# Kernel tuning notes

Measured on AMD Instinct MI355X. Metric: run time of the kernel, lower is better.

The kernel has to match this reference:

```python
import jax, jax.numpy as jnp
import numpy as np
import math


def setup_inputs() -> dict:
    key = jax.random.key(0)
    k1, k2, k3, k4 = jax.random.split(key, 4)
    B, L, H, D = 2, 4096, 8, 64
    factor = 5
    U = factor * int(np.ceil(np.log(L)))  # 45 = sample_k = n_top
    return {
        "queries": jax.random.normal(k1, (B, L, H, D), dtype=jnp.float32),
        "keys": jax.random.normal(k2, (B, L, H, D), dtype=jnp.float32),
        "values": jax.random.normal(k3, (B, L, H, D), dtype=jnp.float32),
        "index_sample": jax.random.randint(k4, (L, U), 0, L),  # sampled key ids per query
    }


def reference(queries, keys, values, index_sample):
    # ProbAttention forward, mask_flag=False (non-causal ProbSparse attention).
    B, L_Q, H, D = queries.shape
    L_K = keys.shape[1]
    Q = jnp.transpose(queries, (0, 2, 1, 3))  # (B,H,L_Q,D)
    K = jnp.transpose(keys, (0, 2, 1, 3))     # (B,H,L_K,D)
    V = jnp.transpose(values, (0, 2, 1, 3))   # (B,H,L_K,D)
    n_top = index_sample.shape[1]             # U = factor*ceil(ln(L_K)) = sample_k = n_top

    # --- _prob_QK: score each query against a random subset of keys ---
    K_sample = K[:, :, index_sample, :]                     # (B,H,L_Q,sample_k,D)
    Q_K_sample = jnp.einsum('bhqd,bhqsd->bhqs', Q, K_sample)
    # sparsity measure M = max - mean (sum divided by full L_K, as in source)
    M = Q_K_sample.max(-1) - Q_K_sample.sum(-1) / L_K       # (B,H,L_Q)
    _, M_top = jax.lax.top_k(M, n_top)                      # (B,H,n_top)

    # full attention scores only for the selected top queries
    Q_reduce = jnp.take_along_axis(Q, M_top[..., None], axis=2)  # (B,H,n_top,D)
    scale = 1.0 / math.sqrt(D)
    scores = jnp.einsum('bhud,bhkd->bhuk', Q_reduce, K) * scale  # (B,H,n_top,L_K)
    attn = jax.nn.softmax(scores, axis=-1)

    # --- initial context (mask_flag=False): cumulative sum of V ---
    context = jnp.cumsum(V, axis=2)                         # (B,H,L_Q,D)

    # --- scatter attention outputs into the top-query rows ---
    update = jnp.einsum('bhuk,bhkd->bhud', attn, V)         # (B,H,n_top,D)
    bi = jnp.arange(B)[:, None, None]
    hi = jnp.arange(H)[None, :, None]
    context = context.at[bi, hi, M_top].set(update)

    return jnp.transpose(context, (0, 2, 1, 3))             # (B,L_Q,H,D)
```

## Files before the change

### kernel.cpp

```cpp
#include <hip/hip_runtime.h>
#include <math.h>

#define BB 2
#define LL 4096
#define HH 8
#define DD 64
#define UU 45
#define TILE 128
#define NTILES (LL / TILE)

#define NC 64
#define CK (LL / NC)
#define KSTR 68
#define SSTR 68

__device__ __forceinline__ int qkv_idx(int b, int l, int h, int d) {
    return ((b * LL + l) * HH + h) * DD + d;
}

__global__ __launch_bounds__(256) void k_computeM(
        const float* __restrict__ Q, const float* __restrict__ K,
        const int* __restrict__ idx, float* __restrict__ M) {
    int w = (blockIdx.x * blockDim.x + threadIdx.x) >> 6;
    int lane = threadIdx.x & 63;
    int q = w % LL;
    int bh = w / LL;
    int h = bh % HH, b = bh / HH;

    const float* Kbh = K + (size_t)(b * LL * HH + h) * DD;
    const size_t rowStride = (size_t)HH * DD;

    float qv = Q[qkv_idx(b, q, h, lane)];
    int myks = idx[q * UU + (lane < UU ? lane : 0)];

    int r = lane >> 4;
    int c16 = lane & 15;

    float q0 = __shfl(qv, c16 * 4 + 0, 64);
    float q1 = __shfl(qv, c16 * 4 + 1, 64);
    float q2 = __shfl(qv, c16 * 4 + 2, 64);
    float q3 = __shfl(qv, c16 * 4 + 3, 64);

    float mval = -INFINITY, sval = 0.f;
#pragma unroll
    for (int g = 0; g < 12; ++g) {
        int s = g * 4 + r;
        int ks = __shfl(myks, s, 64);
        const float4* kp = (const float4*)(Kbh + (size_t)ks * rowStride);
        float4 kk = kp[c16];
        float part = fmaf(kk.x, q0, fmaf(kk.y, q1, fmaf(kk.z, q2, kk.w * q3)));
        part += __shfl_xor(part, 8, 64);
        part += __shfl_xor(part, 4, 64);
        part += __shfl_xor(part, 2, 64);
        part += __shfl_xor(part, 1, 64);
        if (s < UU) { mval = fmaxf(mval, part); sval += part; }
    }
    mval = fmaxf(mval, __shfl_xor(mval, 16, 64));
    sval += __shfl_xor(sval, 16, 64);
    mval = fmaxf(mval, __shfl_xor(mval, 32, 64));
    sval += __shfl_xor(sval, 32, 64);
    if (lane == 0) M[bh * LL + q] = mval - sval * (1.0f / LL);
}

__global__ __launch_bounds__(1024) void k_topk(
        const float* __restrict__ M, int* __restrict__ Mtop) {
    int bh = blockIdx.x;
    int t = threadIdx.x;
    __shared__ unsigned keys[LL];
    __shared__ unsigned hist[256];
    __shared__ unsigned scanbuf[256];
    __shared__ unsigned sPrefix, sMask, sK, sBin;
    __shared__ int outCount, eqCount;
    __shared__ int eqIdx[64];

    for (int i = t; i < LL; i += 1024) {
        unsigned u = __float_as_uint(M[bh * LL + i]);
        keys[i] = (u & 0x80000000u) ? ~u : (u | 0x80000000u);
    }
    if (t == 0) { sPrefix = 0u; sMask = 0u; sK = UU; outCount = 0; eqCount = 0; }
    __syncthreads();

    for (int pass = 0; pass < 4; ++pass) {
        int shift = 24 - pass * 8;
        if (t < 256) hist[t] = 0u;
        __syncthreads();
        unsigned prefix = sPrefix, mask = sMask;
        for (int i = t; i < LL; i += 1024) {
            unsigned k = keys[i];
            if ((k & mask) == prefix)
                atomicAdd(&hist[(k >> shift) & 0xFFu], 1u);
        }
        __syncthreads();
        if (t < 256) scanbuf[t] = hist[t];
        __syncthreads();
        for (int off = 1; off < 256; off <<= 1) {
            unsigned v = 0u;
            if (t < 256 && t + off < 256) v = scanbuf[t + off];
            __syncthreads();
            if (t < 256) scanbuf[t] += v;
            __syncthreads();
        }
        if (t < 256) {
            unsigned k = sK;
            unsigned geq = scanbuf[t];
            unsigned gt = (t < 255) ? scanbuf[t + 1] : 0u;
            if (gt < k && geq >= k) sBin = (unsigned)t;
        }
        __syncthreads();
        if (t == 0) {
            unsigned b = sBin;
            unsigned gt = (b < 255u) ? scanbuf[b + 1] : 0u;
            sK -= gt;
            sPrefix |= (b << shift);
            sMask |= (0xFFu << shift);
        }
        __syncthreads();
    }
    unsigned T = sPrefix;
    int kEq = (int)sK;

    for (int i = t; i < LL; i += 1024) {
        unsigned k = keys[i];
        if (k > T) {
            int slot = atomicAdd(&outCount, 1);
            Mtop[bh * UU + slot] = i;
        } else if (k == T) {
            int e = atomicAdd(&eqCount, 1);
            if (e < 64) eqIdx[e] = i;
        }
    }
    __syncthreads();

    if (t == 0) {
        int base = outCount;
        int ec = eqCount;
        if (ec <= 64) {
            for (int s = 0; s < UU; ++s) {
                if (s >= kEq) break;
                int bi = -1, bv = LL + 2;
                for (int j = 0; j < ec; ++j) {
                    int v = eqIdx[j];
                    if (v < bv) { bv = v; bi = j; }
                }
                Mtop[bh * UU + base + s] = bv;
                eqIdx[bi] = LL + 2;
            }
        } else {
            int got = 0;
            for (int i = 0; i < LL && got < kEq; ++i)
                if (keys[i] == T) { Mtop[bh * UU + base + got] = i; ++got; }
        }
    }
}

__global__ __launch_bounds__(256) void k_tilesum(
        const float* __restrict__ V, float* __restrict__ tsum) {
    int blk = blockIdx.x;
    int tile = blk % NTILES;
    int bh = blk / NTILES;
    int h = bh % HH, b = bh / HH;
    int d = threadIdx.x & 63, g = threadIdx.x >> 6;
    const int CH = TILE / 4;
    int l0 = tile * TILE + g * CH;
    float acc = 0.f;
    for (int i = 0; i < CH; ++i) acc += V[qkv_idx(b, l0 + i, h, d)];
    __shared__ float red[4][DD];
    red[g][d] = acc;
    __syncthreads();
    if (g == 0) tsum[blk * DD + d] = red[0][d] + red[1][d] + red[2][d] + red[3][d];
}

__global__ void k_scantiles(float* __restrict__ tsum) {
    int bh = blockIdx.x;
    int d = threadIdx.x;
    float off = 0.f;
    for (int t = 0; t < NTILES; ++t) {
        int i = (bh * NTILES + t) * DD + d;
        float v = tsum[i];
        tsum[i] = off;
        off += v;
    }
}

__global__ __launch_bounds__(256) void k_cumsum(
        const float* __restrict__ V, const float* __restrict__ tsum,
        float* __restrict__ out) {
    int blk = blockIdx.x;
    int tile = blk % NTILES;
    int bh = blk / NTILES;
    int h = bh % HH, b = bh / HH;
    int d = threadIdx.x & 63, g = threadIdx.x >> 6;
    const int CH = TILE / 4;
    int l0 = tile * TILE + g * CH;

    __shared__ float red[4][DD];
    float acc = 0.f;
    for (int i = 0; i < CH; ++i) acc += V[qkv_idx(b, l0 + i, h, d)];
    red[g][d] = acc;
    __syncthreads();

    float off = tsum[blk * DD + d];
    for (int gg = 0; gg < g; ++gg) off += red[gg][d];

    float run = off;
    for (int i = 0; i < CH; ++i) {
        run += V[qkv_idx(b, l0 + i, h, d)];
        out[qkv_idx(b, l0 + i, h, d)] = run;
    }
}

__global__ __launch_bounds__(256) void k_attn_partial(
        const float* __restrict__ Q, const float* __restrict__ K,
        const float* __restrict__ V, const int* __restrict__ Mtop,
        float* __restrict__ mPart, float* __restrict__ lPart,
        float* __restrict__ Op) {
    int blk = blockIdx.x;
    int c = blk % NC;
    int bh = blk / NC;
    int h = bh % HH, b = bh / HH;
    int k0 = c * CK;
    int t = threadIdx.x;

    __shared__ float Qs[48 * KSTR];
    __shared__ float Ks[CK * KSTR];
    __shared__ float Ss[UU * SSTR];

    const size_t rowStride = (size_t)HH * DD;
    const float* Qbh = Q + (size_t)(b * LL * HH + h) * DD;
    const float* Kbh = K + (size_t)(b * LL * HH + h) * DD;
    const float* Vbh = V + (size_t)(b * LL * HH + h) * DD;

    for (int p = t; p < 48 * DD; p += 256) {
        int u = p >> 6, d = p & 63;
        float v = 0.f;
        if (u < UU) {
            int qi = Mtop[bh * UU + u];
            v = Qbh[(size_t)qi * rowStride + d] * 0.125f;
        }
        Qs[u * KSTR + d] = v;
    }
    for (int p = t; p < CK * 16; p += 256) {
        int row = p >> 4, i = p & 15;
        *(float4*)&Ks[row * KSTR + i * 4] =
            *(const float4*)&Kbh[(size_t)(k0 + row) * rowStride + i * 4];
    }
    __syncthreads();

    int kq = t & 15, uq = t >> 4;
    int u0 = uq * 3;
    float acc[3][4];
#pragma unroll
    for (int i = 0; i < 3; ++i)
#pragma unroll
        for (int j = 0; j < 4; ++j) acc[i][j] = 0.f;

#pragma unroll 4
    for (int dd = 0; dd < 16; ++dd) {
        float4 qf[3];
#pragma unroll
        for (int i = 0; i < 3; ++i)
            qf[i] = *(const float4*)&Qs[(u0 + i) * KSTR + dd * 4];
        float4 kf[4];
#pragma unroll
        for (int j = 0; j < 4; ++j)
            kf[j] = *(const float4*)&Ks[(kq + 16 * j) * KSTR + dd * 4];
#pragma unroll
        for (int i = 0; i < 3; ++i)
#pragma unroll
            for (int j = 0; j < 4; ++j) {
                acc[i][j] = fmaf(qf[i].x, kf[j].x, acc[i][j]);
                acc[i][j] = fmaf(qf[i].y, kf[j].y, acc[i][j]);
                acc[i][j] = fmaf(qf[i].z, kf[j].z, acc[i][j]);
                acc[i][j] = fmaf(qf[i].w, kf[j].w, acc[i][j]);
            }
    }
#pragma unroll
    for (int i = 0; i < 3; ++i) {
        int u = u0 + i;
        if (u < UU)
#pragma unroll
            for (int j = 0; j < 4; ++j) Ss[u * SSTR + kq + 16 * j] = acc[i][j];
    }
    __syncthreads();

    for (int p = t; p < CK * 16; p += 256) {
        int row = p >> 4, i = p & 15;
        *(float4*)&Ks[row * KSTR + i * 4] =
            *(const float4*)&Vbh[(size_t)(k0 + row) * rowStride + i * 4];
    }

    if (t < UU * 4) {
        int u = t >> 2, qq = t & 3;
        float mloc = -INFINITY;
        for (int j = 0; j < CK / 4; ++j)
            mloc = fmaxf(mloc, Ss[u * SSTR + qq + 4 * j]);
        mloc = fmaxf(mloc, __shfl_xor(mloc, 1, 64));
        mloc = fmaxf(mloc, __shfl_xor(mloc, 2, 64));
        float lloc = 0.f;
        for (int j = 0; j < CK / 4; ++j) {
            int kk = qq + 4 * j;
            float e = __expf(Ss[u * SSTR + kk] - mloc);
            Ss[u * SSTR + kk] = e;
            lloc += e;
        }
        lloc += __shfl_xor(lloc, 1, 64);
        lloc += __shfl_xor(lloc, 2, 64);
        if (qq == 0) {
            mPart[(bh * NC + c) * UU + u] = mloc;
            lPart[(bh * NC + c) * UU + u] = lloc;
        }
    }
    __syncthreads();

    int dq = t & 15;
    int d0 = dq * 4;
    if (u0 < UU) {
        float4 o[3];
#pragma unroll
        for (int i = 0; i < 3; ++i) o[i] = make_float4(0.f, 0.f, 0.f, 0.f);
#pragma unroll 4
        for (int kc = 0; kc < CK / 4; ++kc) {
            float4 vk[4];
#pragma unroll
            for (int jj = 0; jj < 4; ++jj)
                vk[jj] = *(const float4*)&Ks[(4 * kc + jj) * KSTR + d0];
#pragma unroll
            for (int i = 0; i < 3; ++i) {
                float4 pf = *(const float4*)&Ss[(u0 + i) * SSTR + 4 * kc];
                o[i].x = fmaf(pf.x, vk[0].x, o[i].x);
                o[i].y = fmaf(pf.x, vk[0].y, o[i].y);
                o[i].z = fmaf(pf.x, vk[0].z, o[i].z);
                o[i].w = fmaf(pf.x, vk[0].w, o[i].w);
                o[i].x = fmaf(pf.y, vk[1].x, o[i].x);
                o[i].y = fmaf(pf.y, vk[1].y, o[i].y);
                o[i].z = fmaf(pf.y, vk[1].z, o[i].z);
                o[i].w = fmaf(pf.y, vk[1].w, o[i].w);
                o[i].x = fmaf(pf.z, vk[2].x, o[i].x);
                o[i].y = fmaf(pf.z, vk[2].y, o[i].y);
                o[i].z = fmaf(pf.z, vk[2].z, o[i].z);
                o[i].w = fmaf(pf.z, vk[2].w, o[i].w);
                o[i].x = fmaf(pf.w, vk[3].x, o[i].x);
                o[i].y = fmaf(pf.w, vk[3].y, o[i].y);
                o[i].z = fmaf(pf.w, vk[3].z, o[i].z);
                o[i].w = fmaf(pf.w, vk[3].w, o[i].w);
            }
        }
#pragma unroll
        for (int i = 0; i < 3; ++i) {
            int u = u0 + i;
            *(float4*)&Op[((size_t)(bh * NC + c) * UU + u) * DD + d0] = o[i];
        }
    }
}

__global__ void k_attn_combine(
        const int* __restrict__ Mtop, const float* __restrict__ mPart,
        const float* __restrict__ lPart, const float* __restrict__ Op,
        float* __restrict__ out) {
    int blk = blockIdx.x;
    int u = blk % UU;
    int bh = blk / UU;
    int h = bh % HH, b = bh / HH;
    int d = threadIdx.x;
    float gm = -INFINITY;
    for (int c = 0; c < NC; ++c)
        gm = fmaxf(gm, mPart[(bh * NC + c) * UU + u]);
    float denom = 0.f, acc = 0.f;
    for (int c = 0; c < NC; ++c) {
        int pi = (bh * NC + c) * UU + u;
        float w = __expf(mPart[pi] - gm);
        denom = fmaf(lPart[pi], w, denom);
        acc = fmaf(w, Op[(size_t)pi * DD + d], acc);
    }
    int qi = Mtop[bh * UU + u];
    out[qkv_idx(b, qi, h, d)] = acc / denom;
}

__global__ __launch_bounds__(256) void k_attn_mono(
        const float* __restrict__ Q, const float* __restrict__ K,
        const float* __restrict__ V, const int* __restrict__ Mtop,
        float* __restrict__ out) {
    int blk = blockIdx.x;
    int u = blk % UU;
    int bh = blk / UU;
    int h = bh % HH, b = bh / HH;
    int qi = Mtop[bh * UU + u];
    int t = threadIdx.x;

    __shared__ float scores[LL];
    __shared__ float red[256];

    const float4* qp = (const float4*)(Q + qkv_idx(b, qi, h, 0));
    float4 qreg[16];
#pragma unroll
    for (int i = 0; i < 16; ++i) {
        float4 v = qp[i];
        v.x *= 0.125f; v.y *= 0.125f; v.z *= 0.125f; v.w *= 0.125f;
        qreg[i] = v;
    }

    float lmax = -INFINITY;
    for (int k = t; k < LL; k += 256) {
        const float4* kr = (const float4*)(K + qkv_idx(b, k, h, 0));
        float dot = 0.f;
#pragma unroll
        for (int i = 0; i < 16; ++i) {
            float4 kk = kr[i];
            dot = fmaf(qreg[i].x, kk.x, dot);
            dot = fmaf(qreg[i].y, kk.y, dot);
            dot = fmaf(qreg[i].z, kk.z, dot);
            dot = fmaf(qreg[i].w, kk.w, dot);
        }
        scores[k] = dot;
        lmax = fmaxf(lmax, dot);
    }
    red[t] = lmax;
    __syncthreads();
    for (int off = 128; off >= 1; off >>= 1) {
        if (t < off) red[t] = fmaxf(red[t], red[t + off]);
        __syncthreads();
    }
    float smax = red[0];
    __syncthreads();

    float lsum = 0.f;
    for (int k = t; k < LL; k += 256) {
        float e = __expf(scores[k] - smax);
        scores[k] = e;
        lsum += e;
    }
    red[t] = lsum;
    __syncthreads();
    for (int off = 128; off >= 1; off >>= 1) {
        if (t < off) red[t] += red[t + off];
        __syncthreads();
    }
    float denom = red[0];
    __syncthreads();

    int d = t & 63, g = t >> 6;
    const float4* sc4 = (const float4*)scores;
    float acc = 0.f;
    for (int kb = g; kb < LL / 4; kb += 4) {
        float4 s4 = sc4[kb];
        int kk0 = kb * 4;
        acc = fmaf(s4.x, V[qkv_idx(b, kk0 + 0, h, d)], acc);
        acc = fmaf(s4.y, V[qkv_idx(b, kk0 + 1, h, d)], acc);
        acc = fmaf(s4.z, V[qkv_idx(b, kk0 + 2, h, d)], acc);
        acc = fmaf(s4.w, V[qkv_idx(b, kk0 + 3, h, d)], acc);
    }
    red[t] = acc;
    __syncthreads();
    if (g == 0) {
        float s = red[d] + red[64 + d] + red[128 + d] + red[192 + d];
        out[qkv_idx(b, qi, h, d)] = s / denom;
    }
}

extern "C" void kernel_launch(void* const* d_in, const int* in_sizes, int n_in,
                              void* d_out, int out_size, void* d_ws, size_t ws_size,
                              hipStream_t stream) {
    const float* Q = (const float*)d_in[0];
    const float* K = (const float*)d_in[1];
    const float* V = (const float*)d_in[2];
    const int* idx = (const int*)d_in[3];
    float* out = (float*)d_out;

    float* ws = (float*)d_ws;

    const size_t M_off = 0;
    const size_t tsum_off = 65536;
    const size_t mP_off = 98304;
    const size_t lP_off = 144384;
    const size_t top_off = 190464;
    const size_t Op_off = 191488;
    const size_t need = (Op_off + (size_t)BB * HH * NC * UU * DD) * 4;

    float* M = ws + M_off;
    float* tsum = ws + tsum_off;

    if (ws_size >= need) {
        float* mPart = ws + mP_off;
        float* lPart = ws + lP_off;
        int* Mtop = (int*)(ws + top_off);
        float* Op = ws + Op_off;

        k_computeM<<<BB * HH * LL / 4, 256, 0, stream>>>(Q, K, idx, M);
        k_topk<<<BB * HH, 1024, 0, stream>>>(M, Mtop);
        k_attn_partial<<<BB * HH * NC, 256, 0, stream>>>(Q, K, V, Mtop,
                                                         mPart, lPart, Op);
        k_tilesum<<<BB * HH * NTILES, 256, 0, stream>>>(V, tsum);
        k_scantiles<<<BB * HH, 64, 0, stream>>>(tsum);
        k_cumsum<<<BB * HH * NTILES, 256, 0, stream>>>(V, tsum, out);
        k_attn_combine<<<BB * HH * UU, 64, 0, stream>>>(Mtop, mPart, lPart,
                                                        Op, out);
    } else {
        int* Mtop = (int*)(ws + 65536);
        float* tsum2 = ws + 65536 + 1024;
        k_computeM<<<BB * HH * LL / 4, 256, 0, stream>>>(Q, K, idx, M);
        k_topk<<<BB * HH, 1024, 0, stream>>>(M, Mtop);
        k_tilesum<<<BB * HH * NTILES, 256, 0, stream>>>(V, tsum2);
        k_scantiles<<<BB * HH, 64, 0, stream>>>(tsum2);
        k_cumsum<<<BB * HH * NTILES, 256, 0, stream>>>(V, tsum2, out);
        k_attn_mono<<<BB * HH * UU, 256, 0, stream>>>(Q, K, V, Mtop, out);
    }
}
```

Baseline: 207.5 us.

## Restructure sparsity-score kernel to one block per query covering all batch-heads

The M computation now assigns one block per query position, where each wavefront handles every batch and head at once: 4 lanes per (b,h) pair, each covering 16 dims. This makes each sampled key row read one contiguous 2 KB span across b/h, instead of one wavefront per (b,h,q) gathering a 256-byte row. The sampled indices are loaded once into shared memory and shared across the 16 batch-head pairs. It also cuts the cross-lane shuffle reduction from 4 steps to 2, but adds two block-level syncs and a shared-memory reduction across the 4 waves.

New measurement: 243.7 us. 1.17x slower.

```diff
diff --git a/kernel.cpp b/kernel.cpp
--- a/kernel.cpp
+++ b/kernel.cpp
@@ -21,45 +21,53 @@
 __global__ __launch_bounds__(256) void k_computeM(
         const float* __restrict__ Q, const float* __restrict__ K,
         const int* __restrict__ idx, float* __restrict__ M) {
-    int w = (blockIdx.x * blockDim.x + threadIdx.x) >> 6;
-    int lane = threadIdx.x & 63;
-    int q = w % LL;
-    int bh = w / LL;
-    int h = bh % HH, b = bh / HH;
-
-    const float* Kbh = K + (size_t)(b * LL * HH + h) * DD;
-    const size_t rowStride = (size_t)HH * DD;
-
-    float qv = Q[qkv_idx(b, q, h, lane)];
-    int myks = idx[q * UU + (lane < UU ? lane : 0)];
-
-    int r = lane >> 4;
-    int c16 = lane & 15;
-
-    float q0 = __shfl(qv, c16 * 4 + 0, 64);
-    float q1 = __shfl(qv, c16 * 4 + 1, 64);
-    float q2 = __shfl(qv, c16 * 4 + 2, 64);
-    float q3 = __shfl(qv, c16 * 4 + 3, 64);
+    int q = blockIdx.x;
+    int t = threadIdx.x;
+    int w = t >> 6, lane = t & 63;
+    int b = lane >> 5, h = (lane >> 2) & 7, c4 = lane & 3;
+
+    __shared__ int sIdx[48];
+    __shared__ float wM[4][16], wS[4][16];
+
+    if (t < 48) sIdx[t] = (t < UU) ? idx[q * UU + t] : 0;
+    __syncthreads();
+
+    const float* qp = Q + qkv_idx(b, q, h, c4 * 16);
+    float4 qf0 = *(const float4*)(qp + 0);
+    float4 qf1 = *(const float4*)(qp + 4);
+    float4 qf2 = *(const float4*)(qp + 8);
+    float4 qf3 = *(const float4*)(qp + 12);
 
     float mval = -INFINITY, sval = 0.f;
-#pragma unroll
-    for (int g = 0; g < 12; ++g) {
-        int s = g * 4 + r;
-        int ks = __shfl(myks, s, 64);
-        const float4* kp = (const float4*)(Kbh + (size_t)ks * rowStride);
-        float4 kk = kp[c16];
-        float part = fmaf(kk.x, q0, fmaf(kk.y, q1, fmaf(kk.z, q2, kk.w * q3)));
-        part += __shfl_xor(part, 8, 64);
-        part += __shfl_xor(part, 4, 64);
-        part += __shfl_xor(part, 2, 64);
-        part += __shfl_xor(part, 1, 64);
-        if (s < UU) { mval = fmaxf(mval, part); sval += part; }
-    }
-    mval = fmaxf(mval, __shfl_xor(mval, 16, 64));
-    sval += __shfl_xor(sval, 16, 64);
-    mval = fmaxf(mval, __shfl_xor(mval, 32, 64));
-    sval += __shfl_xor(sval, 32, 64);
-    if (lane == 0) M[bh * LL + q] = mval - sval * (1.0f / LL);
+#pragma unroll 3
+    for (int si = w; si < 48; si += 4) {
+        int ks = sIdx[si];
+        const float* kp = K + qkv_idx(b, ks, h, c4 * 16);
+        float4 k0 = *(const float4*)(kp + 0);
+        float4 k1 = *(const float4*)(kp + 4);
+        float4 k2 = *(const float4*)(kp + 8);
+        float4 k3 = *(const float4*)(kp + 12);
+        float p = 0.f;
+        p = fmaf(qf0.x, k0.x, p); p = fmaf(qf0.y, k0.y, p);
+        p = fmaf(qf0.z, k0.z, p); p = fmaf(qf0.w, k0.w, p);
+        p = fmaf(qf1.x, k1.x, p); p = fmaf(qf1.y, k1.y, p);
+        p = fmaf(qf1.z, k1.z, p); p = fmaf(qf1.w, k1.w, p);
+        p = fmaf(qf2.x, k2.x, p); p = fmaf(qf2.y, k2.y, p);
+        p = fmaf(qf2.z, k2.z, p); p = fmaf(qf2.w, k2.w, p);
+        p = fmaf(qf3.x, k3.x, p); p = fmaf(qf3.y, k3.y, p);
+        p = fmaf(qf3.z, k3.z, p); p = fmaf(qf3.w, k3.w, p);
+        p += __shfl_xor(p, 1, 64);
+        p += __shfl_xor(p, 2, 64);
+        if (si < UU) { mval = fmaxf(mval, p); sval += p; }
+    }
+    int bh16 = lane >> 2;
+    if (c4 == 0) { wM[w][bh16] = mval; wS[w][bh16] = sval; }
+    __syncthreads();
+    if (t < 16) {
+        float m = fmaxf(fmaxf(wM[0][t], wM[1][t]), fmaxf(wM[2][t], wM[3][t]));
+        float s = wS[0][t] + wS[1][t] + wS[2][t] + wS[3][t];
+        M[t * LL + q] = m - s * (1.0f / LL);
+    }
 }
 
 __global__ __launch_bounds__(1024) void k_topk(
@@ -485,7 +493,7 @@
         int* Mtop = (int*)(ws + top_off);
         float* Op = ws + Op_off;
 
-        k_computeM<<<BB * HH * LL / 4, 256, 0, stream>>>(Q, K, idx, M);
+        k_computeM<<<LL, 256, 0, stream>>>(Q, K, idx, M);
         k_topk<<<BB * HH, 1024, 0, stream>>>(M, Mtop);
         k_attn_partial<<<BB * HH * NC, 256, 0, stream>>>(Q, K, V, Mtop,
                                                          mPart, lPart, Op);
@@ -497,7 +505,7 @@
     } else {
         int* Mtop = (int*)(ws + 65536);
         float* tsum2 = ws + 65536 + 1024;
-        k_computeM<<<BB * HH * LL / 4, 256, 0, stream>>>(Q, K, idx, M);
+        k_computeM<<<LL, 256, 0, stream>>>(Q, K, idx, M);
         k_topk<<<BB * HH, 1024, 0, stream>>>(M, Mtop);
         k_tilesum<<<BB * HH * NTILES, 256, 0, stream>>>(V, tsum2);
         k_scantiles<<<BB * HH, 64, 0, stream>>>(tsum2);
```
